# Kernel tuning notes

Measured on AMD Instinct MI355X. Metric: run time of the kernel, lower is better.

## Reference

```python
import jax, jax.numpy as jnp
import numpy as np

B, N, D_IN, H, MSG, L, TGT, N_LAYERS = 8, 1024, 64, 128, 128, 5, 12, 3


def setup_inputs() -> dict:
    key = jax.random.key(0)
    ks = jax.random.split(key, 10)
    g = jax.random.uniform(ks[0], (B, N, N), jnp.float32)          # adjacency / edge weights
    h_in = jax.random.uniform(ks[1], (B, N, D_IN), jnp.float32)    # node features (positive -> all nodes present)
    e = jax.random.randint(ks[2], (B, N, N), 0, L).astype(jnp.int32)  # discrete edge labels in [0, L)

    def init(k, shape, fan):
        return jax.random.normal(k, shape, jnp.float32) / np.sqrt(fan)

    A = init(ks[3], (L, H, MSG), H)            # per-edge-label message matrices
    Wi = init(ks[4], (MSG, 3 * H), MSG)        # GRU input weights (r,z,n)
    Wh = init(ks[5], (H, 3 * H), H)            # GRU hidden weights (r,z,n)
    bi = jnp.zeros((3 * H,), jnp.float32)
    bh = jnp.zeros((3 * H,), jnp.float32)
    W_gate = init(ks[6], (2 * H, TGT), 2 * H)  # readout gating net i([h_T, h_0])
    b_gate = jnp.zeros((TGT,), jnp.float32)
    W_out = init(ks[7], (H, TGT), H)           # readout net j(h_T)
    b_out = jnp.zeros((TGT,), jnp.float32)
    return dict(g=g, h_in=h_in, e=e, A=A, Wi=Wi, Wh=Wh, bi=bi, bh=bh,
                W_gate=W_gate, b_gate=b_gate, W_out=W_out, b_out=b_out)


def _gru_step(m, h, Wi, Wh, bi, bh):
    # Single GRU step applied independently per node: m [B,N,MSG], h [B,N,H]
    gi = m @ Wi + bi
    gh = h @ Wh + bh
    i_r, i_z, i_n = jnp.split(gi, 3, axis=-1)
    h_r, h_z, h_n = jnp.split(gh, 3, axis=-1)
    r = jax.nn.sigmoid(i_r + h_r)
    z = jax.nn.sigmoid(i_z + h_z)
    n = jnp.tanh(i_n + r * h_n)
    return (1.0 - z) * n + z * h


def reference(g, h_in, e, A, Wi, Wh, bi, bh, W_gate, b_gate, W_out, b_out):
    n_labels, hidden = A.shape[0], A.shape[1]
    # pad input features with zeros up to hidden_state_size
    h0 = jnp.pad(h_in, ((0, 0), (0, 0), (0, hidden - h_in.shape[-1])))
    # node-presence mask: sum(|h_in|) > 0  -> [B,N,1]
    node_mask = (jnp.sum(jnp.abs(h_in), axis=-1, keepdims=True) > 0).astype(h0.dtype)
    h = h0
    for _ in range(N_LAYERS):  # weight-tied message passing
        # per-label candidate messages: M_l[b,w,:] = h[b,w,:] @ A_l  -> [L,B,N,MSG]
        Ml = jnp.einsum('bwd,ldo->lbwo', h, A)
        agg = jnp.zeros(h.shape[:2] + (A.shape[2],), h.dtype)
        for l in range(n_labels):
            # mask by adjacency AND matching edge label, sum over neighbors w
            w_l = g * (e == l).astype(g.dtype)                  # [B,N,N]
            agg = agg + jnp.einsum('bvw,bwo->bvo', w_l, Ml[l])  # [B,N,MSG]
        h = _gru_step(agg, h, Wi, Wh, bi, bh) * node_mask
    hT = h
    # GGNN readout: sum_v sigmoid(i([h_T, h_0])) * j(h_T), masked on present nodes
    gate = jax.nn.sigmoid(jnp.concatenate([hT, h0], axis=-1) @ W_gate + b_gate)
    out = gate * (hT @ W_out + b_out)                            # [B,N,TGT]
    read_mask = (jnp.sum(h0, axis=-1, keepdims=True) > 0).astype(h0.dtype)
    return jnp.sum(out * read_mask, axis=1)                      # [B,TGT]
```

## Files before the change

### kernel.cpp

```cpp
#include <hip/hip_runtime.h>

#define B_      8
#define N_      1024
#define DIN_    64
#define H_      128
#define MSG2    128
#define L_      5
#define TGT_    12
#define NLAYERS_ 3
#define CAT_    640
#define NODES   (B_ * N_)
#define KSPLIT  4

typedef __attribute__((ext_vector_type(8))) short s16x8;
typedef __attribute__((ext_vector_type(4))) float f32x4;

__device__ __forceinline__ float sigmoidf_(float x) { return 1.f / (1.f + __expf(-x)); }

__device__ __forceinline__ unsigned short f2bf(float x) {
  unsigned int u = __float_as_uint(x);
  u += 0x7FFFu + ((u >> 16) & 1u);
  return (unsigned short)(u >> 16);
}
__device__ __forceinline__ float bf2f(unsigned short u) {
  return __uint_as_float(((unsigned int)u) << 16);
}

__global__ __launch_bounds__(256) void k_init(const float* __restrict__ h_in,
                                              float* __restrict__ h,
                                              float* __restrict__ h0,
                                              unsigned short* __restrict__ X,
                                              float* __restrict__ maskA,
                                              float* __restrict__ maskR) {
  int node = blockIdx.x * 4 + (threadIdx.x >> 6);
  int lane = threadIdx.x & 63;
  float v = h_in[(size_t)node * DIN_ + lane];
  size_t base = (size_t)node * H_;
  h[base + lane] = v;   h[base + 64 + lane] = 0.f;
  h0[base + lane] = v;  h0[base + 64 + lane] = 0.f;
  unsigned short hi = f2bf(v);
  unsigned short lo = f2bf(v - bf2f(hi));
  size_t xb = (size_t)node * 256;
  X[xb + lane] = hi;        X[xb + 64 + lane] = 0;
  X[xb + 128 + lane] = lo;  X[xb + 192 + lane] = 0;
  float sa = fabsf(v), ss = v;
  for (int off = 32; off > 0; off >>= 1) {
    sa += __shfl_down(sa, off);
    ss += __shfl_down(ss, off);
  }
  if (lane == 0) {
    maskA[node] = (sa > 0.f) ? 1.f : 0.f;
    maskR[node] = (ss > 0.f) ? 1.f : 0.f;
  }
}

__global__ __launch_bounds__(256) void k_pack(const float* __restrict__ g,
                                              const int* __restrict__ e,
                                              unsigned short* __restrict__ Gb,
                                              unsigned char* __restrict__ Eb) {
  size_t i8 = ((size_t)blockIdx.x * 256 + threadIdx.x) * 8;
  float4 g0 = *(const float4*)&g[i8];
  float4 g1 = *(const float4*)&g[i8 + 4];
  int4   e0 = *(const int4*)&e[i8];
  int4   e1 = *(const int4*)&e[i8 + 4];
  ushort4 ga, gb;
  ga.x = f2bf(g0.x); ga.y = f2bf(g0.y); ga.z = f2bf(g0.z); ga.w = f2bf(g0.w);
  gb.x = f2bf(g1.x); gb.y = f2bf(g1.y); gb.z = f2bf(g1.z); gb.w = f2bf(g1.w);
  *(ushort4*)&Gb[i8]     = ga;
  *(ushort4*)&Gb[i8 + 4] = gb;
  uint2 ev;
  ev.x = (unsigned)(e0.x & 0xFF) | ((unsigned)(e0.y & 0xFF) << 8) |
         ((unsigned)(e0.z & 0xFF) << 16) | ((unsigned)(e0.w & 0xFF) << 24);
  ev.y = (unsigned)(e1.x & 0xFF) | ((unsigned)(e1.y & 0xFF) << 8) |
         ((unsigned)(e1.z & 0xFF) << 16) | ((unsigned)(e1.w & 0xFF) << 24);
  *(uint2*)&Eb[i8] = ev;
}

__global__ __launch_bounds__(256) void k_aprep(const float* __restrict__ A,
                                               unsigned short* __restrict__ ATh,
                                               unsigned short* __restrict__ ATl) {
  int idx = blockIdx.x * 256 + threadIdx.x;
  if (idx >= CAT_ * 128) return;
  int c = idx >> 7, d = idx & 127;
  int l = c >> 7, o = c & 127;
  float v = A[((size_t)l * 128 + d) * 128 + o];
  unsigned short hi = f2bf(v);
  ATh[idx] = hi;
  ATl[idx] = f2bf(v - bf2f(hi));
}

__global__ __launch_bounds__(256) void k_gemmT(const unsigned short* __restrict__ X,
                                               const unsigned short* __restrict__ ATh,
                                               const unsigned short* __restrict__ ATl,
                                               unsigned short* __restrict__ McatT) {
  __shared__ __align__(16) unsigned short Ah[64 * 40];
  __shared__ __align__(16) unsigned short Al[64 * 40];
  __shared__ __align__(16) unsigned short Bh[128 * 40];
  __shared__ __align__(16) unsigned short Bl2[128 * 40];
  const int tid = threadIdx.x;
  const int c0 = blockIdx.x * 128;
  const int node0 = blockIdx.y * 64;
  const int b = node0 >> 10;
  const int w0 = node0 & 1023;
  const int wid = tid >> 6, lane = tid & 63;
  const int wr = wid >> 1, wc = wid & 1;
  const int lr = lane & 15, lg = lane >> 4;
  const int ar = tid >> 2, aq = (tid & 3) * 8;
  const int br = tid >> 1, bq = (tid & 1) * 16;
  f32x4 acc[2][4];
  #pragma unroll
  for (int m = 0; m < 2; ++m)
    #pragma unroll
    for (int n = 0; n < 4; ++n) acc[m][n] = {0.f, 0.f, 0.f, 0.f};
  for (int kk = 0; kk < 4; ++kk) {
    const int kb = kk * 32;
    *(uint4*)&Ah[ar * 40 + aq] = *(const uint4*)&X[(size_t)(node0 + ar) * 256 + kb + aq];
    *(uint4*)&Al[ar * 40 + aq] = *(const uint4*)&X[(size_t)(node0 + ar) * 256 + 128 + kb + aq];
    const unsigned short* bh = ATh + (size_t)(c0 + br) * 128 + kb + bq;
    const unsigned short* bl = ATl + (size_t)(c0 + br) * 128 + kb + bq;
    *(uint4*)&Bh[br * 40 + bq]      = *(const uint4*)bh;
    *(uint4*)&Bh[br * 40 + bq + 8]  = *(const uint4*)(bh + 8);
    *(uint4*)&Bl2[br * 40 + bq]     = *(const uint4*)bl;
    *(uint4*)&Bl2[br * 40 + bq + 8] = *(const uint4*)(bl + 8);
    __syncthreads();
    s16x8 ah[2], al[2], bhf[4], blf[4];
    #pragma unroll
    for (int m = 0; m < 2; ++m) {
      int row = (wr * 32 + m * 16 + lr) * 40 + lg * 8;
      ah[m] = *(const s16x8*)&Ah[row];
      al[m] = *(const s16x8*)&Al[row];
    }
    #pragma unroll
    for (int n = 0; n < 4; ++n) {
      int row = (wc * 64 + n * 16 + lr) * 40 + lg * 8;
      bhf[n] = *(const s16x8*)&Bh[row];
      blf[n] = *(const s16x8*)&Bl2[row];
    }
    #pragma unroll
    for (int m = 0; m < 2; ++m)
      #pragma unroll
      for (int n = 0; n < 4; ++n) {
        acc[m][n] = __builtin_amdgcn_mfma_f32_16x16x32_bf16(ah[m], bhf[n], acc[m][n], 0, 0, 0);
        acc[m][n] = __builtin_amdgcn_mfma_f32_16x16x32_bf16(ah[m], blf[n], acc[m][n], 0, 0, 0);
        acc[m][n] = __builtin_amdgcn_mfma_f32_16x16x32_bf16(al[m], bhf[n], acc[m][n], 0, 0, 0);
      }
    __syncthreads();
  }
  #pragma unroll
  for (int m = 0; m < 2; ++m)
    #pragma unroll
    for (int n = 0; n < 4; ++n) {
      int c = c0 + wc * 64 + n * 16 + lr;
      int l = c >> 7, o = c & 127;
      int w = w0 + wr * 32 + m * 16 + lg * 4;
      ushort4 v;
      v.x = f2bf(acc[m][n][0]); v.y = f2bf(acc[m][n][1]);
      v.z = f2bf(acc[m][n][2]); v.w = f2bf(acc[m][n][3]);
      *(ushort4*)&McatT[(((size_t)b * L_ + l) * MSG2 + o) * N_ + w] = v;
    }
}

__global__ __launch_bounds__(256, 4) void k_agg_mfma(const unsigned short* __restrict__ Gb,
                                                     const unsigned char* __restrict__ Eb,
                                                     const unsigned short* __restrict__ McatT,
                                                     float* __restrict__ aggP) {
  __shared__ __align__(16) unsigned short Gt[64 * 32];
  __shared__ __align__(16) unsigned char  Et[64 * 40];
  __shared__ __align__(16) unsigned short Bl[L_][64 * 32];
  char* GtB = (char*)Gt;
  char* EtB = (char*)Et;
  char* BlB = (char*)Bl;

  const int tid = threadIdx.x;
  const int fid = blockIdx.x;
  const int xcd = fid & 7;
  const int s   = fid >> 3;
  const int p   = xcd * 4 + (s >> 5);
  const int idx = s & 31;
  const int v0  = (idx & 15) * 64;
  const int oh  = idx >> 4;
  const int ks  = p >> 3;
  const int b   = p & 7;

  const int wid  = tid >> 6, lane = tid & 63;
  const int wr   = wid >> 1, wc = wid & 1;
  const int lr   = lane & 15, lg = lane >> 4;

  f32x4 acc[2][2];
  #pragma unroll
  for (int m = 0; m < 2; ++m)
    #pragma unroll
    for (int n = 0; n < 2; ++n) acc[m][n] = {0.f, 0.f, 0.f, 0.f};

  const int ar = tid >> 2, aq = (tid & 3) * 8;
  const int br = tid >> 2, bq = (tid & 3) * 8;
  const size_t garow = ((size_t)b * N_ + v0 + ar) * N_;
  const size_t mrowb = (((size_t)b * L_) * MSG2 + oh * 64 + br) * N_;
  const size_t lstep = (size_t)MSG2 * N_;
  const int ksbase = ks * 256;

  const int gt_w = (ar * 64 + aq * 2) ^ ((ar & 7) << 4);
  const int et_w = ar * 40 + aq;
  const int bl_w = (br * 64 + bq * 2) ^ ((br & 7) << 4);
  const int fsw  = (lr & 7) << 4;

  for (int kk = 0; kk < 8; ++kk) {
    const int kb = ksbase + kk * 32;
    uint4 gv = *(const uint4*)&Gb[garow + kb + aq];
    uint2 ev = *(const uint2*)&Eb[garow + kb + aq];
    uint4 bv[L_];
    #pragma unroll
    for (int l = 0; l < L_; ++l)
      bv[l] = *(const uint4*)(McatT + mrowb + (size_t)l * lstep + kb + bq);
    *(uint4*)(GtB + gt_w) = gv;
    *(uint2*)(EtB + et_w) = ev;
    #pragma unroll
    for (int l = 0; l < L_; ++l)
      *(uint4*)(BlB + l * (64 * 64) + bl_w) = bv[l];
    __syncthreads();

    s16x8 gt[2]; uint2 et[2];
    #pragma unroll
    for (int m = 0; m < 2; ++m) {
      int row = wr * 32 + m * 16 + lr;
      gt[m] = *(const s16x8*)(GtB + ((row * 64 + lg * 16) ^ fsw));
      et[m] = *(const uint2*)(EtB + row * 40 + lg * 8);
    }
    #pragma unroll
    for (int l = 0; l < L_; ++l) {
      s16x8 bfr[2];
      #pragma unroll
      for (int n = 0; n < 2; ++n) {
        int row = wc * 32 + n * 16 + lr;
        bfr[n] = *(const s16x8*)(BlB + l * (64 * 64) + ((row * 64 + lg * 16) ^ fsw));
      }
      #pragma unroll
      for (int m = 0; m < 2; ++m) {
        unsigned int w0e = et[m].x, w1e = et[m].y;
        s16x8 af;
        af[0] = (((w0e      ) & 0xFFu) == (unsigned)l) ? gt[m][0] : (short)0;
        af[1] = (((w0e >>  8) & 0xFFu) == (unsigned)l) ? gt[m][1] : (short)0;
        af[2] = (((w0e >> 16) & 0xFFu) == (unsigned)l) ? gt[m][2] : (short)0;
        af[3] = (((w0e >> 24) & 0xFFu) == (unsigned)l) ? gt[m][3] : (short)0;
        af[4] = (((w1e      ) & 0xFFu) == (unsigned)l) ? gt[m][4] : (short)0;
        af[5] = (((w1e >>  8) & 0xFFu) == (unsigned)l) ? gt[m][5] : (short)0;
        af[6] = (((w1e >> 16) & 0xFFu) == (unsigned)l) ? gt[m][6] : (short)0;
        af[7] = (((w1e >> 24) & 0xFFu) == (unsigned)l) ? gt[m][7] : (short)0;
        #pragma unroll
        for (int n = 0; n < 2; ++n)
          acc[m][n] = __builtin_amdgcn_mfma_f32_16x16x32_bf16(af, bfr[n], acc[m][n], 0, 0, 0);
      }
    }
    __syncthreads();
  }

  float* op = aggP + ((size_t)ks * NODES + (size_t)b * N_ + v0) * MSG2 + oh * 64;
  #pragma unroll
  for (int m = 0; m < 2; ++m)
    #pragma unroll
    for (int n = 0; n < 2; ++n)
      #pragma unroll
      for (int j = 0; j < 4; ++j) {
        int row = wr * 32 + m * 16 + lg * 4 + j;
        int col = wc * 32 + n * 16 + lr;
        op[(size_t)row * MSG2 + col] = acc[m][n][j];
      }
}

__global__ __launch_bounds__(256) void k_xprep(const float* __restrict__ aggP,
                                               float* __restrict__ m) {
  const size_t slab = (size_t)NODES * MSG2;
  size_t i4 = ((size_t)blockIdx.x * 256 + threadIdx.x) * 4;
  float4 s0 = *(const float4*)&aggP[i4];
  float4 s1 = *(const float4*)&aggP[slab + i4];
  float4 s2 = *(const float4*)&aggP[2 * slab + i4];
  float4 s3 = *(const float4*)&aggP[3 * slab + i4];
  float4 s;
  s.x = s0.x + s1.x + s2.x + s3.x;
  s.y = s0.y + s1.y + s2.y + s3.y;
  s.z = s0.z + s1.z + s2.z + s3.z;
  s.w = s0.w + s1.w + s2.w + s3.w;
  *(float4*)&m[i4] = s;
}

__global__ __launch_bounds__(256) void k_gates_f32(const float* __restrict__ m,
                                                   const float* __restrict__ h,
                                                   const float* __restrict__ Wi,
                                                   const float* __restrict__ Wh,
                                                   float* __restrict__ gates) {
  __shared__ float At[32][64];
  __shared__ float Bt[32][64];
  const int z = blockIdx.z;
  const float* X = z ? h : m;
  const float* W = z ? Wh : Wi;
  const int tx = threadIdx.x & 15;
  const int ty = threadIdx.x >> 4;
  const int r0 = blockIdx.y * 64;
  const int c0 = blockIdx.x * 64;
  float acc[4][4] = {};
  const int q    = threadIdx.x * 8;
  const int srow = q >> 5;
  const int sk0  = q & 31;
  const int bk   = threadIdx.x >> 3;
  const int bc   = (threadIdx.x & 7) * 8;
  for (int kc = 0; kc < 128; kc += 32) {
    const float* xs = X + (size_t)(r0 + srow) * 128 + kc + sk0;
    float4 a0 = *(const float4*)xs;
    float4 a1 = *(const float4*)(xs + 4);
    At[sk0+0][srow] = a0.x; At[sk0+1][srow] = a0.y;
    At[sk0+2][srow] = a0.z; At[sk0+3][srow] = a0.w;
    At[sk0+4][srow] = a1.x; At[sk0+5][srow] = a1.y;
    At[sk0+6][srow] = a1.z; At[sk0+7][srow] = a1.w;
    const float* wsrc = W + (size_t)(kc + bk) * 384 + c0 + bc;
    *(float4*)&Bt[bk][bc]     = *(const float4*)wsrc;
    *(float4*)&Bt[bk][bc + 4] = *(const float4*)(wsrc + 4);
    __syncthreads();
    #pragma unroll
    for (int k = 0; k < 32; ++k) {
      float4 av = *(const float4*)&At[k][ty * 4];
      float4 bv = *(const float4*)&Bt[k][tx * 4];
      acc[0][0] += av.x*bv.x; acc[0][1] += av.x*bv.y; acc[0][2] += av.x*bv.z; acc[0][3] += av.x*bv.w;
      acc[1][0] += av.y*bv.x; acc[1][1] += av.y*bv.y; acc[1][2] += av.y*bv.z; acc[1][3] += av.y*bv.w;
      acc[2][0] += av.z*bv.x; acc[2][1] += av.z*bv.y; acc[2][2] += av.z*bv.z; acc[2][3] += av.z*bv.w;
      acc[3][0] += av.w*bv.x; acc[3][1] += av.w*bv.y; acc[3][2] += av.w*bv.z; acc[3][3] += av.w*bv.w;
    }
    __syncthreads();
  }
  #pragma unroll
  for (int i = 0; i < 4; ++i) {
    float4 v = make_float4(acc[i][0], acc[i][1], acc[i][2], acc[i][3]);
    *(float4*)&gates[(size_t)(r0 + ty*4 + i) * 768 + z * 384 + c0 + tx*4] = v;
  }
}

__global__ __launch_bounds__(256) void k_gru_elt(const float* __restrict__ gates,
                                                 const float* __restrict__ bi,
                                                 const float* __restrict__ bh,
                                                 const float* __restrict__ maskA,
                                                 float* __restrict__ h,
                                                 unsigned short* __restrict__ X) {
  const int t = threadIdx.x;
  const int node = blockIdx.x * 8 + (t >> 5);
  const int j4 = (t & 31) * 4;
  const size_t gb = (size_t)node * 768;
  float4 gir = *(const float4*)&gates[gb + j4];
  float4 giz = *(const float4*)&gates[gb + 128 + j4];
  float4 gin = *(const float4*)&gates[gb + 256 + j4];
  float4 ghr = *(const float4*)&gates[gb + 384 + j4];
  float4 ghz = *(const float4*)&gates[gb + 512 + j4];
  float4 ghn = *(const float4*)&gates[gb + 640 + j4];
  float4 bir = *(const float4*)&bi[j4];
  float4 biz = *(const float4*)&bi[128 + j4];
  float4 bin = *(const float4*)&bi[256 + j4];
  float4 bhr = *(const float4*)&bh[j4];
  float4 bhz = *(const float4*)&bh[128 + j4];
  float4 bhn = *(const float4*)&bh[256 + j4];
  float4 hv = *(const float4*)&h[(size_t)node * 128 + j4];
  float m = maskA[node];
  float4 ho;
  {
    float r = sigmoidf_(gir.x + bir.x + ghr.x + bhr.x);
    float z = sigmoidf_(giz.x + biz.x + ghz.x + bhz.x);
    float nn = tanhf(gin.x + bin.x + r * (ghn.x + bhn.x));
    ho.x = ((1.f - z) * nn + z * hv.x) * m;
  }
  {
    float r = sigmoidf_(gir.y + bir.y + ghr.y + bhr.y);
    float z = sigmoidf_(giz.y + biz.y + ghz.y + bhz.y);
    float nn = tanhf(gin.y + bin.y + r * (ghn.y + bhn.y));
    ho.y = ((1.f - z) * nn + z * hv.y) * m;
  }
  {
    float r = sigmoidf_(gir.z + bir.z + ghr.z + bhr.z);
    float z = sigmoidf_(giz.z + biz.z + ghz.z + bhz.z);
    float nn = tanhf(gin.z + bin.z + r * (ghn.z + bhn.z));
    ho.z = ((1.f - z) * nn + z * hv.z) * m;
  }
  {
    float r = sigmoidf_(gir.w + bir.w + ghr.w + bhr.w);
    float z = sigmoidf_(giz.w + biz.w + ghz.w + bhz.w);
    float nn = tanhf(gin.w + bin.w + r * (ghn.w + bhn.w));
    ho.w = ((1.f - z) * nn + z * hv.w) * m;
  }
  *(float4*)&h[(size_t)node * 128 + j4] = ho;
  ushort4 hi, lo;
  hi.x = f2bf(ho.x); lo.x = f2bf(ho.x - bf2f(hi.x));
  hi.y = f2bf(ho.y); lo.y = f2bf(ho.y - bf2f(hi.y));
  hi.z = f2bf(ho.z); lo.z = f2bf(ho.z - bf2f(hi.z));
  hi.w = f2bf(ho.w); lo.w = f2bf(ho.w - bf2f(hi.w));
  *(ushort4*)&X[(size_t)node * 256 + j4]       = hi;
  *(ushort4*)&X[(size_t)node * 256 + 128 + j4] = lo;
}

__global__ __launch_bounds__(256) void k_readP(const float* __restrict__ h,
                                               const float* __restrict__ h0,
                                               const float* __restrict__ Wg,
                                               const float* __restrict__ Wo,
                                               float* __restrict__ PT) {
  __shared__ float Xt[64][65];
  __shared__ float Wt[64][25];
  const int tid = threadIdx.x;
  const int node0 = blockIdx.x * 64;
  const int row = tid >> 2;
  const int cg  = tid & 3;
  float acc[6] = {0.f, 0.f, 0.f, 0.f, 0.f, 0.f};
  const int sr = tid >> 2;
  const int sk = (tid & 3) * 16;
  #pragma unroll
  for (int kb = 0; kb < 4; ++kb) {
    const float* src = (kb < 2 ? h : h0) + (size_t)(node0 + sr) * 128 + (kb & 1) * 64 + sk;
    #pragma unroll
    for (int q = 0; q < 4; ++q)
      *(float4*)&Xt[sr][sk + q * 4] = *(const float4*)(src + q * 4);
    #pragma unroll
    for (int j = 0; j < 6; ++j) {
      int idx = tid * 6 + j;
      int rk = idx / 24;
      int c24 = idx - rk * 24;
      int gk = kb * 64 + rk;
      float wv;
      if (c24 < 12) wv = Wg[(size_t)gk * TGT_ + c24];
      else          wv = (gk < 128) ? Wo[(size_t)gk * TGT_ + (c24 - 12)] : 0.f;
      Wt[rk][c24] = wv;
    }
    __syncthreads();
    #pragma unroll 8
    for (int k = 0; k < 64; ++k) {
      float x = Xt[row][k];
      #pragma unroll
      for (int j = 0; j < 6; ++j)
        acc[j] += x * Wt[k][cg * 6 + j];
    }
    __syncthreads();
  }
  #pragma unroll
  for (int j = 0; j < 6; ++j)
    PT[(size_t)(cg * 6 + j) * NODES + node0 + row] = acc[j];
}

__global__ __launch_bounds__(256) void k_readR(const float* __restrict__ PT,
                                               const float* __restrict__ maskR,
                                               const float* __restrict__ bg,
                                               const float* __restrict__ bo,
                                               float* __restrict__ out) {
  __shared__ float red[256];
  const int tid = threadIdx.x;
  const int b = blockIdx.x / TGT_;
  const int t = blockIdx.x - b * TGT_;
  const float bgt = bg[t], bot = bo[t];
  float s = 0.f;
  #pragma unroll
  for (int i = 0; i < 4; ++i) {
    int node = b * N_ + i * 256 + tid;
    float p1 = PT[(size_t)t * NODES + node] + bgt;
    float p2 = PT[(size_t)(12 + t) * NODES + node] + bot;
    s += sigmoidf_(p1) * p2 * maskR[node];
  }
  red[tid] = s;
  __syncthreads();
  #pragma unroll
  for (int off = 128; off > 0; off >>= 1) {
    if (tid < off) red[tid] += red[tid + off];
    __syncthreads();
  }
  if (tid == 0) out[b * TGT_ + t] = red[0];
}

extern "C" void kernel_launch(void* const* d_in, const int* in_sizes, int n_in,
                              void* d_out, int out_size, void* d_ws, size_t ws_size,
                              hipStream_t stream) {
  (void)in_sizes; (void)n_in; (void)out_size; (void)ws_size;
  const float* g    = (const float*)d_in[0];
  const float* h_in = (const float*)d_in[1];
  const int*   e    = (const int*)d_in[2];
  const float* A    = (const float*)d_in[3];
  const float* Wi   = (const float*)d_in[4];
  const float* Wh   = (const float*)d_in[5];
  const float* bi   = (const float*)d_in[6];
  const float* bh   = (const float*)d_in[7];
  const float* Wg   = (const float*)d_in[8];
  const float* bg   = (const float*)d_in[9];
  const float* Wo   = (const float*)d_in[10];
  const float* bo   = (const float*)d_in[11];
  float* out = (float*)d_out;
  float* ws  = (float*)d_ws;

  float* h     = ws;
  float* h0    = h + (size_t)NODES * H_;
  float* maskA = h0 + (size_t)NODES * H_;
  float* maskR = maskA + NODES;
  float* m     = maskR + NODES;
  unsigned short* X   = (unsigned short*)(m + (size_t)NODES * MSG2);
  unsigned short* ATh = X + (size_t)NODES * 256;
  unsigned short* ATl = ATh + CAT_ * 128;
  unsigned short* Gb  = ATl + CAT_ * 128;
  unsigned char*  Eb  = (unsigned char*)(Gb + (size_t)NODES * N_);
  float* aggP = (float*)(Eb + (size_t)NODES * N_);
  unsigned short* McatT = (unsigned short*)(aggP + (size_t)KSPLIT * NODES * MSG2);
  float* gates = aggP;
  float* PT = m;

  k_init<<<NODES / 4, 256, 0, stream>>>(h_in, h, h0, X, maskA, maskR);
  k_pack<<<(NODES * N_ / 8) / 256, 256, 0, stream>>>(g, e, Gb, Eb);
  k_aprep<<<(CAT_ * 128 + 255) / 256, 256, 0, stream>>>(A, ATh, ATl);
  for (int layer = 0; layer < NLAYERS_; ++layer) {
    k_gemmT<<<dim3(CAT_ / 128, NODES / 64), 256, 0, stream>>>(X, ATh, ATl, McatT);
    k_agg_mfma<<<(N_ / 64) * 2 * KSPLIT * B_, 256, 0, stream>>>(Gb, Eb, McatT, aggP);
    k_xprep<<<(NODES * MSG2 / 4) / 256, 256, 0, stream>>>(aggP, m);
    k_gates_f32<<<dim3(384 / 64, NODES / 64, 2), 256, 0, stream>>>(m, h, Wi, Wh, gates);
    k_gru_elt<<<NODES / 8, 256, 0, stream>>>(gates, bi, bh, maskA, h, X);
  }
  k_readP<<<NODES / 64, 256, 0, stream>>>(h, h0, Wg, Wo, PT);
  k_readR<<<B_ * TGT_, 256, 0, stream>>>(PT, maskR, bg, bo, out);
}
```

Before: 257.7 us.

## Move GRU gate GEMMs to split-bf16 MFMA and prefetch agg tiles

Replaces the fp32 FMA gate GEMM with a bf16 MFMA kernel that uses hi/lo split operands (three MFMAs per tile) to keep near-fp32 accuracy. The Wi/Wh weights are pre-transposed and split once, and the k-split reduction now writes bf16 hi/lo messages directly. Separately, the aggregation kernel register-prefetches the next k-tile of G, E and M while computing the current one. The aim is to cut scalar FMA cost in the gate GEMMs and hide global load latency in aggregation, at the cost of more registers and an extra prep kernel.

```diff
diff --git a/kernel.cpp b/kernel.cpp
--- a/kernel.cpp
+++ b/kernel.cpp
@@ -89,6 +89,27 @@
   ATl[idx] = f2bf(v - bf2f(hi));
 }
 
+__global__ __launch_bounds__(256) void k_wprep(const float* __restrict__ Wi,
+                                               const float* __restrict__ Wh,
+                                               unsigned short* __restrict__ WiTh,
+                                               unsigned short* __restrict__ WiTl,
+                                               unsigned short* __restrict__ WhTh,
+                                               unsigned short* __restrict__ WhTl) {
+  int idx = blockIdx.x * 256 + threadIdx.x;
+  if (idx < 384 * 128) {
+    int c = idx >> 7, k = idx & 127;
+    float v = Wi[(size_t)k * 384 + c];
+    unsigned short hi = f2bf(v);
+    WiTh[idx] = hi; WiTl[idx] = f2bf(v - bf2f(hi));
+  } else if (idx < 2 * 384 * 128) {
+    int i = idx - 384 * 128;
+    int c = i >> 7, k = i & 127;
+    float v = Wh[(size_t)k * 384 + c];
+    unsigned short hi = f2bf(v);
+    WhTh[i] = hi; WhTl[i] = f2bf(v - bf2f(hi));
+  }
+}
+
 __global__ __launch_bounds__(256) void k_gemmT(const unsigned short* __restrict__ X,
                                                const unsigned short* __restrict__ ATh,
                                                const unsigned short* __restrict__ ATl,
@@ -204,20 +225,32 @@
   const int bl_w = (br * 64 + bq * 2) ^ ((br & 7) << 4);
   const int fsw  = (lr & 7) << 4;
 
-  for (int kk = 0; kk < 8; ++kk) {
-    const int kb = ksbase + kk * 32;
-    uint4 gv = *(const uint4*)&Gb[garow + kb + aq];
-    uint2 ev = *(const uint2*)&Eb[garow + kb + aq];
-    uint4 bv[L_];
+  uint4 gv; uint2 ev; uint4 bv[L_];
+  {
+    const int kb = ksbase;
+    gv = *(const uint4*)&Gb[garow + kb + aq];
+    ev = *(const uint2*)&Eb[garow + kb + aq];
     #pragma unroll
     for (int l = 0; l < L_; ++l)
       bv[l] = *(const uint4*)(McatT + mrowb + (size_t)l * lstep + kb + bq);
+  }
+
+  for (int kk = 0; kk < 8; ++kk) {
     *(uint4*)(GtB + gt_w) = gv;
     *(uint2*)(EtB + et_w) = ev;
     #pragma unroll
     for (int l = 0; l < L_; ++l)
       *(uint4*)(BlB + l * (64 * 64) + bl_w) = bv[l];
     __syncthreads();
+
+    if (kk < 7) {
+      const int kb = ksbase + (kk + 1) * 32;
+      gv = *(const uint4*)&Gb[garow + kb + aq];
+      ev = *(const uint2*)&Eb[garow + kb + aq];
+      #pragma unroll
+      for (int l = 0; l < L_; ++l)
+        bv[l] = *(const uint4*)(McatT + mrowb + (size_t)l * lstep + kb + bq);
+    }
 
     s16x8 gt[2]; uint2 et[2];
     #pragma unroll
@@ -268,7 +301,7 @@
 }
 
 __global__ __launch_bounds__(256) void k_xprep(const float* __restrict__ aggP,
-                                               float* __restrict__ m) {
+                                               unsigned short* __restrict__ Xm) {
   const size_t slab = (size_t)NODES * MSG2;
   size_t i4 = ((size_t)blockIdx.x * 256 + threadIdx.x) * 4;
   float4 s0 = *(const float4*)&aggP[i4];
@@ -280,57 +313,89 @@
   s.y = s0.y + s1.y + s2.y + s3.y;
   s.z = s0.z + s1.z + s2.z + s3.z;
   s.w = s0.w + s1.w + s2.w + s3.w;
-  *(float4*)&m[i4] = s;
-}
-
-__global__ __launch_bounds__(256) void k_gates_f32(const float* __restrict__ m,
-                                                   const float* __restrict__ h,
-                                                   const float* __restrict__ Wi,
-                                                   const float* __restrict__ Wh,
-                                                   float* __restrict__ gates) {
-  __shared__ float At[32][64];
-  __shared__ float Bt[32][64];
+  size_t node = i4 >> 7;
+  size_t j = i4 & 127;
+  ushort4 hi, lo;
+  hi.x = f2bf(s.x); lo.x = f2bf(s.x - bf2f(hi.x));
+  hi.y = f2bf(s.y); lo.y = f2bf(s.y - bf2f(hi.y));
+  hi.z = f2bf(s.z); lo.z = f2bf(s.z - bf2f(hi.z));
+  hi.w = f2bf(s.w); lo.w = f2bf(s.w - bf2f(hi.w));
+  *(ushort4*)&Xm[node * 256 + j]       = hi;
+  *(ushort4*)&Xm[node * 256 + 128 + j] = lo;
+}
+
+__global__ __launch_bounds__(256) void k_gates_mfma(const unsigned short* __restrict__ Xm,
+                                                    const unsigned short* __restrict__ Xh,
+                                                    const unsigned short* __restrict__ WiTh,
+                                                    const unsigned short* __restrict__ WiTl,
+                                                    const unsigned short* __restrict__ WhTh,
+                                                    const unsigned short* __restrict__ WhTl,
+                                                    float* __restrict__ gates) {
+  __shared__ __align__(16) unsigned short Ah[64 * 40];
+  __shared__ __align__(16) unsigned short Al[64 * 40];
+  __shared__ __align__(16) unsigned short Bh[128 * 40];
+  __shared__ __align__(16) unsigned short Bl2[128 * 40];
+  const int tid = threadIdx.x;
   const int z = blockIdx.z;
-  const float* X = z ? h : m;
-  const float* W = z ? Wh : Wi;
-  const int tx = threadIdx.x & 15;
-  const int ty = threadIdx.x >> 4;
-  const int r0 = blockIdx.y * 64;
-  const int c0 = blockIdx.x * 64;
-  float acc[4][4] = {};
-  const int q    = threadIdx.x * 8;
-  const int srow = q >> 5;
-  const int sk0  = q & 31;
-  const int bk   = threadIdx.x >> 3;
-  const int bc   = (threadIdx.x & 7) * 8;
-  for (int kc = 0; kc < 128; kc += 32) {
-    const float* xs = X + (size_t)(r0 + srow) * 128 + kc + sk0;
-    float4 a0 = *(const float4*)xs;
-    float4 a1 = *(const float4*)(xs + 4);
-    At[sk0+0][srow] = a0.x; At[sk0+1][srow] = a0.y;
-    At[sk0+2][srow] = a0.z; At[sk0+3][srow] = a0.w;
-    At[sk0+4][srow] = a1.x; At[sk0+5][srow] = a1.y;
-    At[sk0+6][srow] = a1.z; At[sk0+7][srow] = a1.w;
-    const float* wsrc = W + (size_t)(kc + bk) * 384 + c0 + bc;
-    *(float4*)&Bt[bk][bc]     = *(const float4*)wsrc;
-    *(float4*)&Bt[bk][bc + 4] = *(const float4*)(wsrc + 4);
-    __syncthreads();
-    #pragma unroll
-    for (int k = 0; k < 32; ++k) {
-      float4 av = *(const float4*)&At[k][ty * 4];
-      float4 bv = *(const float4*)&Bt[k][tx * 4];
-      acc[0][0] += av.x*bv.x; acc[0][1] += av.x*bv.y; acc[0][2] += av.x*bv.z; acc[0][3] += av.x*bv.w;
-      acc[1][0] += av.y*bv.x; acc[1][1] += av.y*bv.y; acc[1][2] += av.y*bv.z; acc[1][3] += av.y*bv.w;
-      acc[2][0] += av.z*bv.x; acc[2][1] += av.z*bv.y; acc[2][2] += av.z*bv.z; acc[2][3] += av.z*bv.w;
-      acc[3][0] += av.w*bv.x; acc[3][1] += av.w*bv.y; acc[3][2] += av.w*bv.z; acc[3][3] += av.w*bv.w;
-    }
-    __syncthreads();
-  }
-  #pragma unroll
-  for (int i = 0; i < 4; ++i) {
-    float4 v = make_float4(acc[i][0], acc[i][1], acc[i][2], acc[i][3]);
-    *(float4*)&gates[(size_t)(r0 + ty*4 + i) * 768 + z * 384 + c0 + tx*4] = v;
-  }
+  const unsigned short* Xp  = z ? Xh : Xm;
+  const unsigned short* WTh = z ? WhTh : WiTh;
+  const unsigned short* WTl = z ? WhTl : WiTl;
+  const int c0 = blockIdx.x * 128;
+  const int node0 = blockIdx.y * 64;
+  const int wid = tid >> 6, lane = tid & 63;
+  const int wr = wid >> 1, wc = wid & 1;
+  const int lr = lane & 15, lg = lane >> 4;
+  const int ar = tid >> 2, aq = (tid & 3) * 8;
+  const int br = tid >> 1, bq = (tid & 1) * 16;
+  f32x4 acc[2][4];
+  #pragma unroll
+  for (int m = 0; m < 2; ++m)
+    #pragma unroll
+    for (int n = 0; n < 4; ++n) acc[m][n] = {0.f, 0.f, 0.f, 0.f};
+  for (int kk = 0; kk < 4; ++kk) {
+    const int kb = kk * 32;
+    *(uint4*)&Ah[ar * 40 + aq] = *(const uint4*)&Xp[(size_t)(node0 + ar) * 256 + kb + aq];
+    *(uint4*)&Al[ar * 40 + aq] = *(const uint4*)&Xp[(size_t)(node0 + ar) * 256 + 128 + kb + aq];
+    const unsigned short* bh = WTh + (size_t)(c0 + br) * 128 + kb + bq;
+    const unsigned short* bl = WTl + (size_t)(c0 + br) * 128 + kb + bq;
+    *(uint4*)&Bh[br * 40 + bq]      = *(const uint4*)bh;
+    *(uint4*)&Bh[br * 40 + bq + 8]  = *(const uint4*)(bh + 8);
+    *(uint4*)&Bl2[br * 40 + bq]     = *(const uint4*)bl;
+    *(uint4*)&Bl2[br * 40 + bq + 8] = *(const uint4*)(bl + 8);
+    __syncthreads();
+    s16x8 ah[2], al[2], bhf[4], blf[4];
+    #pragma unroll
+    for (int m = 0; m < 2; ++m) {
+      int row = (wr * 32 + m * 16 + lr) * 40 + lg * 8;
+      ah[m] = *(const s16x8*)&Ah[row];
+      al[m] = *(const s16x8*)&Al[row];
+    }
+    #pragma unroll
+    for (int n = 0; n < 4; ++n) {
+      int row = (wc * 64 + n * 16 + lr) * 40 + lg * 8;
+      bhf[n] = *(const s16x8*)&Bh[row];
+      blf[n] = *(const s16x8*)&Bl2[row];
+    }
+    #pragma unroll
+    for (int m = 0; m < 2; ++m)
+      #pragma unroll
+      for (int n = 0; n < 4; ++n) {
+        acc[m][n] = __builtin_amdgcn_mfma_f32_16x16x32_bf16(ah[m], bhf[n], acc[m][n], 0, 0, 0);
+        acc[m][n] = __builtin_amdgcn_mfma_f32_16x16x32_bf16(ah[m], blf[n], acc[m][n], 0, 0, 0);
+        acc[m][n] = __builtin_amdgcn_mfma_f32_16x16x32_bf16(al[m], bhf[n], acc[m][n], 0, 0, 0);
+      }
+    __syncthreads();
+  }
+  #pragma unroll
+  for (int m = 0; m < 2; ++m)
+    #pragma unroll
+    for (int n = 0; n < 4; ++n) {
+      int c = c0 + wc * 64 + n * 16 + lr;
+      int row = node0 + wr * 32 + m * 16 + lg * 4;
+      #pragma unroll
+      for (int j = 0; j < 4; ++j)
+        gates[(size_t)(row + j) * 768 + z * 384 + c] = acc[m][n][j];
+    }
 }
 
 __global__ __launch_bounds__(256) void k_gru_elt(const float* __restrict__ gates,
@@ -489,25 +554,30 @@
   float* h0    = h + (size_t)NODES * H_;
   float* maskA = h0 + (size_t)NODES * H_;
   float* maskR = maskA + NODES;
-  float* m     = maskR + NODES;
-  unsigned short* X   = (unsigned short*)(m + (size_t)NODES * MSG2);
-  unsigned short* ATh = X + (size_t)NODES * 256;
-  unsigned short* ATl = ATh + CAT_ * 128;
-  unsigned short* Gb  = ATl + CAT_ * 128;
-  unsigned char*  Eb  = (unsigned char*)(Gb + (size_t)NODES * N_);
+  unsigned short* X    = (unsigned short*)(maskR + NODES);
+  unsigned short* Xm   = X + (size_t)NODES * 256;
+  unsigned short* ATh  = Xm + (size_t)NODES * 256;
+  unsigned short* ATl  = ATh + CAT_ * 128;
+  unsigned short* WiTh = ATl + CAT_ * 128;
+  unsigned short* WiTl = WiTh + 384 * 128;
+  unsigned short* WhTh = WiTl + 384 * 128;
+  unsigned short* WhTl = WhTh + 384 * 128;
+  unsigned short* Gb   = WhTl + 384 * 128;
+  unsigned char*  Eb   = (unsigned char*)(Gb + (size_t)NODES * N_);
   float* aggP = (float*)(Eb + (size_t)NODES * N_);
   unsigned short* McatT = (unsigned short*)(aggP + (size_t)KSPLIT * NODES * MSG2);
   float* gates = aggP;
-  float* PT = m;
+  float* PT = (float*)Xm;
 
   k_init<<<NODES / 4, 256, 0, stream>>>(h_in, h, h0, X, maskA, maskR);
   k_pack<<<(NODES * N_ / 8) / 256, 256, 0, stream>>>(g, e, Gb, Eb);
   k_aprep<<<(CAT_ * 128 + 255) / 256, 256, 0, stream>>>(A, ATh, ATl);
+  k_wprep<<<(2 * 384 * 128 + 255) / 256, 256, 0, stream>>>(Wi, Wh, WiTh, WiTl, WhTh, WhTl);
   for (int layer = 0; layer < NLAYERS_; ++layer) {
     k_gemmT<<<dim3(CAT_ / 128, NODES / 64), 256, 0, stream>>>(X, ATh, ATl, McatT);
     k_agg_mfma<<<(N_ / 64) * 2 * KSPLIT * B_, 256, 0, stream>>>(Gb, Eb, McatT, aggP);
-    k_xprep<<<(NODES * MSG2 / 4) / 256, 256, 0, stream>>>(aggP, m);
-    k_gates_f32<<<dim3(384 / 64, NODES / 64, 2), 256, 0, stream>>>(m, h, Wi, Wh, gates);
+    k_xprep<<<(NODES * MSG2 / 4) / 256, 256, 0, stream>>>(aggP, Xm);
+    k_gates_mfma<<<dim3(384 / 128, NODES / 64, 2), 256, 0, stream>>>(Xm, X, WiTh, WiTl, WhTh, WhTl, gates);
     k_gru_elt<<<NODES / 8, 256, 0, stream>>>(gates, bi, bh, maskA, h, X);
   }
   k_readP<<<NODES / 64, 256, 0, stream>>>(h, h0, Wg, Wo, PT);
```

Measured after the change: 321.8 us. +24.9%, slower.
